# Performance work log

Measured on AMD Instinct MI355X. Metric: run time of the kernel, lower is better.

Reference implementation:

```python
import jax, jax.numpy as jnp
import numpy as np

OH, OW = 32, 32          # adaptive pool output size
NUM_KERNELS = 2
LATENT = 100             # latent_dims = [100, 100]
S = (OH // 2) * (OW // 2)  # in_spatial = 256


def adaptive_avg_pool(x, oh, ow):
    # exact-divisor adaptive avg pool == block mean
    B, C, H, W = x.shape
    return x.reshape(B, C, oh, H // oh, ow, W // ow).mean(axis=(3, 5))


def setup_inputs() -> dict:
    key = jax.random.key(0)
    k1, k2, k3, k4 = jax.random.split(key, 4)
    x = jax.random.normal(k1, (8, 512, 128, 128), dtype=jnp.float32)
    scale = 1.0 / np.sqrt(S)
    psi_w = jax.random.normal(k2, (NUM_KERNELS, S, LATENT), dtype=jnp.float32) * scale  # visible->latent proj
    phi_w = jax.random.normal(k3, (NUM_KERNELS, S, LATENT), dtype=jnp.float32) * scale  # latent->visible proj
    out_w = jax.random.normal(k4, (S, S), dtype=jnp.float32) * scale                    # output linear over spatial feats
    return {"x": x, "psi_w": psi_w, "phi_w": phi_w, "out_w": out_w}


def reference(x, psi_w, phi_w, out_w):
    B, C, H, W = x.shape
    # GAP: adaptive average pool to (OH, OW)
    xg = adaptive_avg_pool(x, OH, OW)                                   # [B,C,32,32]
    # internal 2x2 avg pool (accounts for in_spatial = h/2 * ceil(w/2))
    v = xg.reshape(B, C, OH // 2, 2, OW // 2, 2).mean(axis=(3, 5))
    v = v.reshape(B, C, S)                                              # channel nodes [B,C,S]
    # visible -> latent affinity (softmax over visible/channel nodes)
    A_v2l = jax.nn.softmax(jnp.einsum('bcs,ksd->bkdc', v, psi_w), axis=-1)  # [B,K,d1,C]
    z = jnp.einsum('bkdc,bcs->bkds', A_v2l, v).reshape(B, NUM_KERNELS * LATENT, S)  # [B,Kd1,S]
    # latent -> latent propagation on normalized features
    zn = z / (jnp.linalg.norm(z, axis=-1, keepdims=True) + 1e-6)
    G = jax.nn.softmax(jnp.einsum('bms,bns->bmn', zn, zn), axis=-1)     # [B,Kd1,Kd1]
    zp = jnp.einsum('bmn,bns->bms', G, z).reshape(B, NUM_KERNELS, LATENT, S)
    # latent -> visible affinity (softmax over latent nodes)
    A_l2v = jax.nn.softmax(jnp.einsum('bcs,ksd->bkcd', v, phi_w), axis=-1)  # [B,K,C,d2]
    out = jnp.einsum('bkcd,bkds->bcs', A_l2v, zp)                       # [B,C,S]
    out = jnp.einsum('bcs,st->bct', out, out_w)
    f = v + out                                                          # residual
    attn = jax.nn.sigmoid(f.mean(axis=-1))                               # [B,C]
    return attn[:, :, None, None]                                        # [B,C,1,1]
```

## Files before the change

kernel.cpp:

```cpp
#include <hip/hip_runtime.h>
#include <math.h>

constexpr int Bn = 8, Cn = 512, Sn = 256, Mn = 200, Ln = 100;

constexpr size_t OFF_V    = 0;
constexpr size_t OFF_Z    = OFF_V   + (size_t)Bn*Cn*Sn;
constexpr size_t OFF_INV  = OFF_Z   + (size_t)Bn*Mn*Sn;
constexpr size_t OFF_ZW   = OFF_INV + (size_t)Bn*Mn;
constexpr size_t OFF_ZPW  = OFF_ZW  + (size_t)Bn*Mn;
constexpr size_t OFF_WSUM = OFF_ZPW + (size_t)Bn*Mn;

template<int NW>
__device__ __forceinline__ float4 blk_max_f4(float4 x, float4* red) {
  #pragma unroll
  for (int o = 32; o; o >>= 1) {
    x.x = fmaxf(x.x, __shfl_xor(x.x, o));
    x.y = fmaxf(x.y, __shfl_xor(x.y, o));
    x.z = fmaxf(x.z, __shfl_xor(x.z, o));
    x.w = fmaxf(x.w, __shfl_xor(x.w, o));
  }
  __syncthreads();
  if ((threadIdx.x & 63) == 0) red[threadIdx.x >> 6] = x;
  __syncthreads();
  float4 r = red[0];
  #pragma unroll
  for (int w = 1; w < NW; ++w) {
    r.x = fmaxf(r.x, red[w].x); r.y = fmaxf(r.y, red[w].y);
    r.z = fmaxf(r.z, red[w].z); r.w = fmaxf(r.w, red[w].w);
  }
  return r;
}
template<int NW>
__device__ __forceinline__ float4 blk_sum_f4(float4 x, float4* red) {
  #pragma unroll
  for (int o = 32; o; o >>= 1) {
    x.x += __shfl_xor(x.x, o); x.y += __shfl_xor(x.y, o);
    x.z += __shfl_xor(x.z, o); x.w += __shfl_xor(x.w, o);
  }
  __syncthreads();
  if ((threadIdx.x & 63) == 0) red[threadIdx.x >> 6] = x;
  __syncthreads();
  float4 r = red[0];
  #pragma unroll
  for (int w = 1; w < NW; ++w) {
    r.x += red[w].x; r.y += red[w].y; r.z += red[w].z; r.w += red[w].w;
  }
  return r;
}

__global__ void __launch_bounds__(256) k_pool(const float* __restrict__ x,
                                              const float* __restrict__ ow,
                                              float* __restrict__ ws) {
  int t = threadIdx.x;
  if (blockIdx.x == 4096) {
    const float* row = ow + (size_t)t * Sn;
    float s = 0.f;
    for (int j = 0; j < Sn; j += 4) {
      float4 f = *(const float4*)(row + j);
      s += f.x + f.y + f.z + f.w;
    }
    ws[OFF_WSUM + t] = s;
    return;
  }
  int bc = blockIdx.x;
  const float* plane = x + (size_t)bc * 16384;
  float part[16];
  #pragma unroll
  for (int i = 0; i < 16; ++i) {
    float4 f = *(const float4*)(plane + i * 1024 + t * 4);
    part[i] = f.x + f.y + f.z + f.w;
  }
  __shared__ float lds[256][17];
  #pragma unroll
  for (int i = 0; i < 16; ++i) lds[t][i] = part[i];
  __syncthreads();
  int i = t >> 4, jj = t & 15;
  float s = 0.f;
  #pragma unroll
  for (int r = 0; r < 8; ++r)
    s += lds[32 * r + 2 * jj][i] + lds[32 * r + 2 * jj + 1][i];
  ws[OFF_V + (size_t)bc * 256 + t] = s * (1.0f / 64.0f);
}

__global__ void __launch_bounds__(512) k_psz(const float* __restrict__ psi,
                                             float* __restrict__ ws) {
  int b = blockIdx.y, g = blockIdx.x, t = threadIdx.x;
  int m0 = g * 8;
  __shared__ __align__(16) float pc[8][256];
  __shared__ __align__(16) float As[8][512];
  __shared__ __align__(16) float zpart[2][8][256];
  __shared__ float4 red4[8];
  const float* v = ws + OFF_V + (size_t)b * Cn * Sn;

  for (int e = t; e < 8 * 256; e += 512) {
    int mm = e >> 8, s = e & 255;
    int m = m0 + mm, k = m / Ln, d = m % Ln;
    pc[mm][s] = psi[(size_t)k * Sn * Ln + (size_t)s * Ln + d];
  }
  __syncthreads();

  float acc[8] = {0, 0, 0, 0, 0, 0, 0, 0};
  {
    const float* vp = v + (size_t)t * Sn;
    for (int s = 0; s < Sn; s += 4) {
      float4 vv = *(const float4*)(vp + s);
      #pragma unroll
      for (int mm = 0; mm < 8; ++mm) {
        float4 p = *(const float4*)&pc[mm][s];
        acc[mm] += vv.x * p.x + vv.y * p.y + vv.z * p.z + vv.w * p.w;
      }
    }
  }
  #pragma unroll
  for (int q = 0; q < 2; ++q) {
    float4 a = make_float4(acc[4*q], acc[4*q+1], acc[4*q+2], acc[4*q+3]);
    float4 mx = blk_max_f4<8>(a, red4);
    float4 e;
    e.x = expf(a.x - mx.x); e.y = expf(a.y - mx.y);
    e.z = expf(a.z - mx.z); e.w = expf(a.w - mx.w);
    float4 se = blk_sum_f4<8>(e, red4);
    As[4*q+0][t] = e.x / se.x;
    As[4*q+1][t] = e.y / se.y;
    As[4*q+2][t] = e.z / se.z;
    As[4*q+3][t] = e.w / se.w;
  }
  __syncthreads();

  int h = t >> 8, s2 = t & 255;
  float a2[8] = {0, 0, 0, 0, 0, 0, 0, 0};
  const float* vb = v + (size_t)h * 256 * Sn;
  for (int c = 0; c < 256; c += 4) {
    float v0 = vb[(size_t)(c + 0) * Sn + s2];
    float v1 = vb[(size_t)(c + 1) * Sn + s2];
    float v2 = vb[(size_t)(c + 2) * Sn + s2];
    float v3 = vb[(size_t)(c + 3) * Sn + s2];
    #pragma unroll
    for (int mm = 0; mm < 8; ++mm) {
      float4 aa = *(const float4*)&As[mm][h * 256 + c];
      a2[mm] += aa.x * v0 + aa.y * v1 + aa.z * v2 + aa.w * v3;
    }
  }
  #pragma unroll
  for (int mm = 0; mm < 8; ++mm) zpart[h][mm][s2] = a2[mm];
  __syncthreads();

  float zv[8] = {0, 0, 0, 0, 0, 0, 0, 0};
  float wsv = 0.f;
  if (t < 256) {
    wsv = ws[OFF_WSUM + t];
    float* zo = ws + OFF_Z + ((size_t)b * Mn + m0) * Sn;
    #pragma unroll
    for (int mm = 0; mm < 8; ++mm) {
      zv[mm] = zpart[0][mm][t] + zpart[1][mm][t];
      zo[(size_t)mm * Sn + t] = zv[mm];
    }
  }
  #pragma unroll
  for (int q = 0; q < 2; ++q) {
    float4 sq = make_float4(zv[4*q]*zv[4*q], zv[4*q+1]*zv[4*q+1],
                            zv[4*q+2]*zv[4*q+2], zv[4*q+3]*zv[4*q+3]);
    float4 n2 = blk_sum_f4<8>(sq, red4);
    float4 zw = blk_sum_f4<8>(make_float4(zv[4*q]*wsv, zv[4*q+1]*wsv,
                                          zv[4*q+2]*wsv, zv[4*q+3]*wsv), red4);
    if (t == 0) {
      float* inv = ws + OFF_INV + (size_t)b * Mn + m0 + 4*q;
      float* zwp = ws + OFF_ZW  + (size_t)b * Mn + m0 + 4*q;
      inv[0] = 1.0f / (sqrtf(n2.x) + 1e-6f); zwp[0] = zw.x;
      inv[1] = 1.0f / (sqrtf(n2.y) + 1e-6f); zwp[1] = zw.y;
      inv[2] = 1.0f / (sqrtf(n2.z) + 1e-6f); zwp[2] = zw.z;
      inv[3] = 1.0f / (sqrtf(n2.w) + 1e-6f); zwp[3] = zw.w;
    }
  }
}

__global__ void __launch_bounds__(256) k_g(float* __restrict__ ws) {
  int b = blockIdx.y, g = blockIdx.x, t = threadIdx.x;
  int m0 = g * 4;
  __shared__ __align__(16) float zl[4][256];
  __shared__ float invl[200], zwl[200];
  __shared__ float4 red4[4];
  const float* z = ws + OFF_Z + (size_t)b * Mn * Sn;
  #pragma unroll
  for (int mm = 0; mm < 4; ++mm) zl[mm][t] = z[(size_t)(m0 + mm) * Sn + t];
  if (t < Mn) {
    invl[t] = ws[OFF_INV + (size_t)b * Mn + t];
    zwl[t]  = ws[OFF_ZW  + (size_t)b * Mn + t];
  }
  __syncthreads();
  bool act = t < Mn;
  float dot[4] = {0, 0, 0, 0};
  if (act) {
    const float* zr = z + (size_t)t * Sn;
    for (int s = 0; s < Sn; s += 4) {
      float4 zz = *(const float4*)(zr + s);
      #pragma unroll
      for (int mm = 0; mm < 4; ++mm) {
        float4 zl4 = *(const float4*)&zl[mm][s];
        dot[mm] += zz.x * zl4.x + zz.y * zl4.y + zz.z * zl4.z + zz.w * zl4.w;
      }
    }
  }
  float4 val;
  val.x = act ? dot[0] * invl[m0 + 0] * invl[t] : -1e30f;
  val.y = act ? dot[1] * invl[m0 + 1] * invl[t] : -1e30f;
  val.z = act ? dot[2] * invl[m0 + 2] * invl[t] : -1e30f;
  val.w = act ? dot[3] * invl[m0 + 3] * invl[t] : -1e30f;
  float4 mx = blk_max_f4<4>(val, red4);
  float4 e;
  e.x = act ? expf(val.x - mx.x) : 0.f;
  e.y = act ? expf(val.y - mx.y) : 0.f;
  e.z = act ? expf(val.z - mx.z) : 0.f;
  e.w = act ? expf(val.w - mx.w) : 0.f;
  float4 se = blk_sum_f4<4>(e, red4);
  float zwn = act ? zwl[t] : 0.f;
  float4 sez = blk_sum_f4<4>(make_float4(e.x*zwn, e.y*zwn, e.z*zwn, e.w*zwn), red4);
  if (t == 0) {
    float* zp = ws + OFF_ZPW + (size_t)b * Mn + m0;
    zp[0] = sez.x / se.x; zp[1] = sez.y / se.y;
    zp[2] = sez.z / se.z; zp[3] = sez.w / se.w;
  }
}

__global__ void __launch_bounds__(256) k_out(const float* __restrict__ phi,
                                             float* __restrict__ out,
                                             float* __restrict__ ws) {
  int b = blockIdx.y, cg = blockIdx.x, t = threadIdx.x;
  int c0 = cg * 8;
  __shared__ __align__(16) float vl[8][256];
  __shared__ float zpl[200];
  __shared__ float t2l[16][104];
  __shared__ float resl[2][8];
  __shared__ float vsl[8];
  const float* v = ws + OFF_V + ((size_t)b * Cn + c0) * Sn;
  #pragma unroll
  for (int cc = 0; cc < 8; ++cc) vl[cc][t] = v[(size_t)cc * Sn + t];
  if (t < Mn) zpl[t] = ws[OFF_ZPW + (size_t)b * Mn + t];
  __syncthreads();
  int k = t >> 7, d = t & 127;
  int dd = d < Ln ? d : Ln - 1;
  const float* pp = phi + (size_t)k * Sn * Ln + dd;
  float acc[8] = {0, 0, 0, 0, 0, 0, 0, 0};
  for (int s = 0; s < Sn; s += 4) {
    float p0 = pp[(size_t)(s + 0) * Ln];
    float p1 = pp[(size_t)(s + 1) * Ln];
    float p2 = pp[(size_t)(s + 2) * Ln];
    float p3 = pp[(size_t)(s + 3) * Ln];
    #pragma unroll
    for (int cc = 0; cc < 8; ++cc) {
      float4 vv = *(const float4*)&vl[cc][s];
      acc[cc] += vv.x * p0 + vv.y * p1 + vv.z * p2 + vv.w * p3;
    }
  }
  if (d < Ln) {
    #pragma unroll
    for (int cc = 0; cc < 8; ++cc) t2l[k * 8 + cc][d] = acc[cc];
  }
  __syncthreads();
  int gg = t >> 4, l = t & 15;
  int k2 = gg >> 3, cc2 = gg & 7;
  float mx = -1e30f;
  for (int dq = l; dq < Ln; dq += 16) mx = fmaxf(mx, t2l[gg][dq]);
  #pragma unroll
  for (int o = 8; o; o >>= 1) mx = fmaxf(mx, __shfl_xor(mx, o));
  float se = 0.f, sez = 0.f;
  for (int dq = l; dq < Ln; dq += 16) {
    float e = expf(t2l[gg][dq] - mx);
    se += e;
    sez += e * zpl[k2 * Ln + dq];
  }
  #pragma unroll
  for (int o = 8; o; o >>= 1) { se += __shfl_xor(se, o); sez += __shfl_xor(sez, o); }
  float vs = 0.f;
  if (k2 == 0) {
    for (int i2 = 0; i2 < 16; ++i2) vs += vl[cc2][i2 * 16 + l];
    #pragma unroll
    for (int o = 8; o; o >>= 1) vs += __shfl_xor(vs, o);
    if (l == 0) vsl[cc2] = vs;
  }
  if (l == 0) resl[k2][cc2] = sez / se;
  __syncthreads();
  if (t < 8) {
    float f = (vsl[t] + resl[0][t] + resl[1][t]) * (1.0f / 256.0f);
    out[(size_t)b * Cn + c0 + t] = 1.0f / (1.0f + expf(-f));
  }
}

extern "C" void kernel_launch(void* const* d_in, const int* in_sizes, int n_in,
                              void* d_out, int out_size, void* d_ws, size_t ws_size,
                              hipStream_t stream) {
  const float* x   = (const float*)d_in[0];
  const float* psi = (const float*)d_in[1];
  const float* phi = (const float*)d_in[2];
  const float* ow  = (const float*)d_in[3];
  float* out = (float*)d_out;
  float* ws  = (float*)d_ws;

  hipLaunchKernelGGL(k_pool, dim3(4097),   dim3(256), 0, stream, x, ow, ws);
  hipLaunchKernelGGL(k_psz,  dim3(25, 8),  dim3(512), 0, stream, psi, ws);
  hipLaunchKernelGGL(k_g,    dim3(50, 8),  dim3(256), 0, stream, ws);
  hipLaunchKernelGGL(k_out,  dim3(64, 8),  dim3(256), 0, stream, phi, out, ws);
}
```

Before: 125.8 us.

## Add transposed v and z copies for coalesced loads and halve per-block work

The pooling kernel now also writes a transposed copy of v (S×C) and interleaves its block order across batches. k_psz writes a transposed z copy, and k_psz and k_g read these transposed buffers so each thread's loads are coalesced across lanes instead of strided per-thread rows. k_psz, k_g and k_out each handle half as many rows per block, doubling grid sizes for more parallelism. In exchange there are extra scattered global writes for the transposes and more total loads of the shared operands.

```diff
diff --git a/kernel.cpp b/kernel.cpp
--- a/kernel.cpp
+++ b/kernel.cpp
@@ -4,8 +4,10 @@
 constexpr int Bn = 8, Cn = 512, Sn = 256, Mn = 200, Ln = 100;
 
 constexpr size_t OFF_V    = 0;
-constexpr size_t OFF_Z    = OFF_V   + (size_t)Bn*Cn*Sn;
-constexpr size_t OFF_INV  = OFF_Z   + (size_t)Bn*Mn*Sn;
+constexpr size_t OFF_VT   = OFF_V   + (size_t)Bn*Cn*Sn;
+constexpr size_t OFF_Z    = OFF_VT  + (size_t)Bn*Sn*Cn;
+constexpr size_t OFF_ZT   = OFF_Z   + (size_t)Bn*Mn*Sn;
+constexpr size_t OFF_INV  = OFF_ZT  + (size_t)Bn*Sn*Mn;
 constexpr size_t OFF_ZW   = OFF_INV + (size_t)Bn*Mn;
 constexpr size_t OFF_ZPW  = OFF_ZW  + (size_t)Bn*Mn;
 constexpr size_t OFF_WSUM = OFF_ZPW + (size_t)Bn*Mn;
@@ -62,7 +64,8 @@
     ws[OFF_WSUM + t] = s;
     return;
   }
-  int bc = blockIdx.x;
+  int orig = blockIdx.x;
+  int bc = (orig & 7) * 512 + (orig >> 3);
   const float* plane = x + (size_t)bc * 16384;
   float part[16];
   #pragma unroll
@@ -79,145 +82,142 @@
   #pragma unroll
   for (int r = 0; r < 8; ++r)
     s += lds[32 * r + 2 * jj][i] + lds[32 * r + 2 * jj + 1][i];
-  ws[OFF_V + (size_t)bc * 256 + t] = s * (1.0f / 64.0f);
+  float val = s * (1.0f / 64.0f);
+  ws[OFF_V + (size_t)bc * 256 + t] = val;
+  int b = bc >> 9, c = bc & 511;
+  ws[OFF_VT + ((size_t)b * Sn + t) * Cn + c] = val;
 }
 
 __global__ void __launch_bounds__(512) k_psz(const float* __restrict__ psi,
                                              float* __restrict__ ws) {
   int b = blockIdx.y, g = blockIdx.x, t = threadIdx.x;
-  int m0 = g * 8;
-  __shared__ __align__(16) float pc[8][256];
-  __shared__ __align__(16) float As[8][512];
-  __shared__ __align__(16) float zpart[2][8][256];
+  int m0 = g * 4;
+  __shared__ __align__(16) float pc[4][256];
+  __shared__ __align__(16) float As[4][512];
+  __shared__ __align__(16) float zpart[2][4][256];
   __shared__ float4 red4[8];
-  const float* v = ws + OFF_V + (size_t)b * Cn * Sn;
-
-  for (int e = t; e < 8 * 256; e += 512) {
+  const float* v  = ws + OFF_V  + (size_t)b * Cn * Sn;
+  const float* vT = ws + OFF_VT + (size_t)b * Sn * Cn;
+
+  for (int e = t; e < 4 * 256; e += 512) {
     int mm = e >> 8, s = e & 255;
     int m = m0 + mm, k = m / Ln, d = m % Ln;
     pc[mm][s] = psi[(size_t)k * Sn * Ln + (size_t)s * Ln + d];
   }
   __syncthreads();
 
-  float acc[8] = {0, 0, 0, 0, 0, 0, 0, 0};
+  float acc[4] = {0, 0, 0, 0};
+  for (int s = 0; s < Sn; s += 4) {
+    float v0 = vT[(size_t)(s + 0) * Cn + t];
+    float v1 = vT[(size_t)(s + 1) * Cn + t];
+    float v2 = vT[(size_t)(s + 2) * Cn + t];
+    float v3 = vT[(size_t)(s + 3) * Cn + t];
+    #pragma unroll
+    for (int mm = 0; mm < 4; ++mm) {
+      float4 p = *(const float4*)&pc[mm][s];
+      acc[mm] += v0 * p.x + v1 * p.y + v2 * p.z + v3 * p.w;
+    }
+  }
   {
-    const float* vp = v + (size_t)t * Sn;
-    for (int s = 0; s < Sn; s += 4) {
-      float4 vv = *(const float4*)(vp + s);
-      #pragma unroll
-      for (int mm = 0; mm < 8; ++mm) {
-        float4 p = *(const float4*)&pc[mm][s];
-        acc[mm] += vv.x * p.x + vv.y * p.y + vv.z * p.z + vv.w * p.w;
-      }
-    }
-  }
-  #pragma unroll
-  for (int q = 0; q < 2; ++q) {
-    float4 a = make_float4(acc[4*q], acc[4*q+1], acc[4*q+2], acc[4*q+3]);
+    float4 a = make_float4(acc[0], acc[1], acc[2], acc[3]);
     float4 mx = blk_max_f4<8>(a, red4);
     float4 e;
     e.x = expf(a.x - mx.x); e.y = expf(a.y - mx.y);
     e.z = expf(a.z - mx.z); e.w = expf(a.w - mx.w);
     float4 se = blk_sum_f4<8>(e, red4);
-    As[4*q+0][t] = e.x / se.x;
-    As[4*q+1][t] = e.y / se.y;
-    As[4*q+2][t] = e.z / se.z;
-    As[4*q+3][t] = e.w / se.w;
+    As[0][t] = e.x / se.x;
+    As[1][t] = e.y / se.y;
+    As[2][t] = e.z / se.z;
+    As[3][t] = e.w / se.w;
   }
   __syncthreads();
 
   int h = t >> 8, s2 = t & 255;
-  float a2[8] = {0, 0, 0, 0, 0, 0, 0, 0};
+  float a2[4] = {0, 0, 0, 0};
   const float* vb = v + (size_t)h * 256 * Sn;
   for (int c = 0; c < 256; c += 4) {
-    float v0 = vb[(size_t)(c + 0) * Sn + s2];
-    float v1 = vb[(size_t)(c + 1) * Sn + s2];
-    float v2 = vb[(size_t)(c + 2) * Sn + s2];
-    float v3 = vb[(size_t)(c + 3) * Sn + s2];
-    #pragma unroll
-    for (int mm = 0; mm < 8; ++mm) {
+    float w0 = vb[(size_t)(c + 0) * Sn + s2];
+    float w1 = vb[(size_t)(c + 1) * Sn + s2];
+    float w2 = vb[(size_t)(c + 2) * Sn + s2];
+    float w3 = vb[(size_t)(c + 3) * Sn + s2];
+    #pragma unroll
+    for (int mm = 0; mm < 4; ++mm) {
       float4 aa = *(const float4*)&As[mm][h * 256 + c];
-      a2[mm] += aa.x * v0 + aa.y * v1 + aa.z * v2 + aa.w * v3;
-    }
-  }
-  #pragma unroll
-  for (int mm = 0; mm < 8; ++mm) zpart[h][mm][s2] = a2[mm];
-  __syncthreads();
-
-  float zv[8] = {0, 0, 0, 0, 0, 0, 0, 0};
+      a2[mm] += aa.x * w0 + aa.y * w1 + aa.z * w2 + aa.w * w3;
+    }
+  }
+  #pragma unroll
+  for (int mm = 0; mm < 4; ++mm) zpart[h][mm][s2] = a2[mm];
+  __syncthreads();
+
+  float zv[4] = {0, 0, 0, 0};
   float wsv = 0.f;
   if (t < 256) {
     wsv = ws[OFF_WSUM + t];
     float* zo = ws + OFF_Z + ((size_t)b * Mn + m0) * Sn;
     #pragma unroll
-    for (int mm = 0; mm < 8; ++mm) {
+    for (int mm = 0; mm < 4; ++mm) {
       zv[mm] = zpart[0][mm][t] + zpart[1][mm][t];
       zo[(size_t)mm * Sn + t] = zv[mm];
     }
-  }
-  #pragma unroll
-  for (int q = 0; q < 2; ++q) {
-    float4 sq = make_float4(zv[4*q]*zv[4*q], zv[4*q+1]*zv[4*q+1],
-                            zv[4*q+2]*zv[4*q+2], zv[4*q+3]*zv[4*q+3]);
-    float4 n2 = blk_sum_f4<8>(sq, red4);
-    float4 zw = blk_sum_f4<8>(make_float4(zv[4*q]*wsv, zv[4*q+1]*wsv,
-                                          zv[4*q+2]*wsv, zv[4*q+3]*wsv), red4);
-    if (t == 0) {
-      float* inv = ws + OFF_INV + (size_t)b * Mn + m0 + 4*q;
-      float* zwp = ws + OFF_ZW  + (size_t)b * Mn + m0 + 4*q;
-      inv[0] = 1.0f / (sqrtf(n2.x) + 1e-6f); zwp[0] = zw.x;
-      inv[1] = 1.0f / (sqrtf(n2.y) + 1e-6f); zwp[1] = zw.y;
-      inv[2] = 1.0f / (sqrtf(n2.z) + 1e-6f); zwp[2] = zw.z;
-      inv[3] = 1.0f / (sqrtf(n2.w) + 1e-6f); zwp[3] = zw.w;
-    }
+    *(float4*)&ws[OFF_ZT + ((size_t)b * Sn + t) * Mn + m0] =
+        make_float4(zv[0], zv[1], zv[2], zv[3]);
+  }
+  float4 n2 = blk_sum_f4<8>(make_float4(zv[0]*zv[0], zv[1]*zv[1],
+                                        zv[2]*zv[2], zv[3]*zv[3]), red4);
+  float4 zw = blk_sum_f4<8>(make_float4(zv[0]*wsv, zv[1]*wsv,
+                                        zv[2]*wsv, zv[3]*wsv), red4);
+  if (t == 0) {
+    float* inv = ws + OFF_INV + (size_t)b * Mn + m0;
+    float* zwp = ws + OFF_ZW  + (size_t)b * Mn + m0;
+    inv[0] = 1.0f / (sqrtf(n2.x) + 1e-6f); zwp[0] = zw.x;
+    inv[1] = 1.0f / (sqrtf(n2.y) + 1e-6f); zwp[1] = zw.y;
+    inv[2] = 1.0f / (sqrtf(n2.z) + 1e-6f); zwp[2] = zw.z;
+    inv[3] = 1.0f / (sqrtf(n2.w) + 1e-6f); zwp[3] = zw.w;
   }
 }
 
 __global__ void __launch_bounds__(256) k_g(float* __restrict__ ws) {
   int b = blockIdx.y, g = blockIdx.x, t = threadIdx.x;
-  int m0 = g * 4;
-  __shared__ __align__(16) float zl[4][256];
+  int m0 = g * 2;
+  __shared__ __align__(16) float zl[2][256];
   __shared__ float invl[200], zwl[200];
   __shared__ float4 red4[4];
-  const float* z = ws + OFF_Z + (size_t)b * Mn * Sn;
-  #pragma unroll
-  for (int mm = 0; mm < 4; ++mm) zl[mm][t] = z[(size_t)(m0 + mm) * Sn + t];
+  const float* z  = ws + OFF_Z  + (size_t)b * Mn * Sn;
+  const float* zT = ws + OFF_ZT + (size_t)b * Sn * Mn;
+  zl[0][t] = z[(size_t)(m0 + 0) * Sn + t];
+  zl[1][t] = z[(size_t)(m0 + 1) * Sn + t];
   if (t < Mn) {
     invl[t] = ws[OFF_INV + (size_t)b * Mn + t];
     zwl[t]  = ws[OFF_ZW  + (size_t)b * Mn + t];
   }
   __syncthreads();
   bool act = t < Mn;
-  float dot[4] = {0, 0, 0, 0};
+  float d0 = 0.f, d1 = 0.f;
   if (act) {
-    const float* zr = z + (size_t)t * Sn;
     for (int s = 0; s < Sn; s += 4) {
-      float4 zz = *(const float4*)(zr + s);
-      #pragma unroll
-      for (int mm = 0; mm < 4; ++mm) {
-        float4 zl4 = *(const float4*)&zl[mm][s];
-        dot[mm] += zz.x * zl4.x + zz.y * zl4.y + zz.z * zl4.z + zz.w * zl4.w;
-      }
+      float z0 = zT[(size_t)(s + 0) * Mn + t];
+      float z1 = zT[(size_t)(s + 1) * Mn + t];
+      float z2 = zT[(size_t)(s + 2) * Mn + t];
+      float z3 = zT[(size_t)(s + 3) * Mn + t];
+      d0 += z0 * zl[0][s] + z1 * zl[0][s+1] + z2 * zl[0][s+2] + z3 * zl[0][s+3];
+      d1 += z0 * zl[1][s] + z1 * zl[1][s+1] + z2 * zl[1][s+2] + z3 * zl[1][s+3];
     }
   }
   float4 val;
-  val.x = act ? dot[0] * invl[m0 + 0] * invl[t] : -1e30f;
-  val.y = act ? dot[1] * invl[m0 + 1] * invl[t] : -1e30f;
-  val.z = act ? dot[2] * invl[m0 + 2] * invl[t] : -1e30f;
-  val.w = act ? dot[3] * invl[m0 + 3] * invl[t] : -1e30f;
+  val.x = act ? d0 * invl[m0 + 0] * invl[t] : -1e30f;
+  val.y = act ? d1 * invl[m0 + 1] * invl[t] : -1e30f;
+  val.z = -1e30f; val.w = -1e30f;
   float4 mx = blk_max_f4<4>(val, red4);
-  float4 e;
-  e.x = act ? expf(val.x - mx.x) : 0.f;
-  e.y = act ? expf(val.y - mx.y) : 0.f;
-  e.z = act ? expf(val.z - mx.z) : 0.f;
-  e.w = act ? expf(val.w - mx.w) : 0.f;
-  float4 se = blk_sum_f4<4>(e, red4);
+  float ex = act ? expf(val.x - mx.x) : 0.f;
+  float ey = act ? expf(val.y - mx.y) : 0.f;
+  float4 se = blk_sum_f4<4>(make_float4(ex, ey, 0.f, 0.f), red4);
   float zwn = act ? zwl[t] : 0.f;
-  float4 sez = blk_sum_f4<4>(make_float4(e.x*zwn, e.y*zwn, e.z*zwn, e.w*zwn), red4);
+  float4 sez = blk_sum_f4<4>(make_float4(ex * zwn, ey * zwn, 0.f, 0.f), red4);
   if (t == 0) {
     float* zp = ws + OFF_ZPW + (size_t)b * Mn + m0;
-    zp[0] = sez.x / se.x; zp[1] = sez.y / se.y;
-    zp[2] = sez.z / se.z; zp[3] = sez.w / se.w;
+    zp[0] = sez.x / se.x;
+    zp[1] = sez.y / se.y;
   }
 }
 
@@ -225,61 +225,61 @@
                                              float* __restrict__ out,
                                              float* __restrict__ ws) {
   int b = blockIdx.y, cg = blockIdx.x, t = threadIdx.x;
-  int c0 = cg * 8;
-  __shared__ __align__(16) float vl[8][256];
+  int c0 = cg * 4;
+  __shared__ __align__(16) float vl[4][256];
   __shared__ float zpl[200];
-  __shared__ float t2l[16][104];
-  __shared__ float resl[2][8];
-  __shared__ float vsl[8];
+  __shared__ float t2l[8][104];
+  __shared__ float resl[2][4];
+  __shared__ float vsl[4];
   const float* v = ws + OFF_V + ((size_t)b * Cn + c0) * Sn;
   #pragma unroll
-  for (int cc = 0; cc < 8; ++cc) vl[cc][t] = v[(size_t)cc * Sn + t];
+  for (int cc = 0; cc < 4; ++cc) vl[cc][t] = v[(size_t)cc * Sn + t];
   if (t < Mn) zpl[t] = ws[OFF_ZPW + (size_t)b * Mn + t];
   __syncthreads();
   int k = t >> 7, d = t & 127;
   int dd = d < Ln ? d : Ln - 1;
   const float* pp = phi + (size_t)k * Sn * Ln + dd;
-  float acc[8] = {0, 0, 0, 0, 0, 0, 0, 0};
+  float acc[4] = {0, 0, 0, 0};
   for (int s = 0; s < Sn; s += 4) {
     float p0 = pp[(size_t)(s + 0) * Ln];
     float p1 = pp[(size_t)(s + 1) * Ln];
     float p2 = pp[(size_t)(s + 2) * Ln];
     float p3 = pp[(size_t)(s + 3) * Ln];
     #pragma unroll
-    for (int cc = 0; cc < 8; ++cc) {
+    for (int cc = 0; cc < 4; ++cc) {
       float4 vv = *(const float4*)&vl[cc][s];
       acc[cc] += vv.x * p0 + vv.y * p1 + vv.z * p2 + vv.w * p3;
     }
   }
   if (d < Ln) {
     #pragma unroll
-    for (int cc = 0; cc < 8; ++cc) t2l[k * 8 + cc][d] = acc[cc];
-  }
-  __syncthreads();
-  int gg = t >> 4, l = t & 15;
-  int k2 = gg >> 3, cc2 = gg & 7;
+    for (int cc = 0; cc < 4; ++cc) t2l[k * 4 + cc][d] = acc[cc];
+  }
+  __syncthreads();
+  int gg = t >> 5, l = t & 31;
+  int k2 = gg >> 2, cc2 = gg & 3;
   float mx = -1e30f;
-  for (int dq = l; dq < Ln; dq += 16) mx = fmaxf(mx, t2l[gg][dq]);
-  #pragma unroll
-  for (int o = 8; o; o >>= 1) mx = fmaxf(mx, __shfl_xor(mx, o));
+  for (int dq = l; dq < Ln; dq += 32) mx = fmaxf(mx, t2l[gg][dq]);
+  #pragma unroll
+  for (int o = 16; o; o >>= 1) mx = fmaxf(mx, __shfl_xor(mx, o));
   float se = 0.f, sez = 0.f;
-  for (int dq = l; dq < Ln; dq += 16) {
+  for (int dq = l; dq < Ln; dq += 32) {
     float e = expf(t2l[gg][dq] - mx);
     se += e;
     sez += e * zpl[k2 * Ln + dq];
   }
   #pragma unroll
-  for (int o = 8; o; o >>= 1) { se += __shfl_xor(se, o); sez += __shfl_xor(sez, o); }
+  for (int o = 16; o; o >>= 1) { se += __shfl_xor(se, o); sez += __shfl_xor(sez, o); }
   float vs = 0.f;
   if (k2 == 0) {
-    for (int i2 = 0; i2 < 16; ++i2) vs += vl[cc2][i2 * 16 + l];
-    #pragma unroll
-    for (int o = 8; o; o >>= 1) vs += __shfl_xor(vs, o);
+    for (int i2 = 0; i2 < 8; ++i2) vs += vl[cc2][i2 * 32 + l];
+    #pragma unroll
+    for (int o = 16; o; o >>= 1) vs += __shfl_xor(vs, o);
     if (l == 0) vsl[cc2] = vs;
   }
   if (l == 0) resl[k2][cc2] = sez / se;
   __syncthreads();
-  if (t < 8) {
+  if (t < 4) {
     float f = (vsl[t] + resl[0][t] + resl[1][t]) * (1.0f / 256.0f);
     out[(size_t)b * Cn + c0 + t] = 1.0f / (1.0f + expf(-f));
   }
@@ -295,8 +295,8 @@
   float* out = (float*)d_out;
   float* ws  = (float*)d_ws;
 
-  hipLaunchKernelGGL(k_pool, dim3(4097),   dim3(256), 0, stream, x, ow, ws);
-  hipLaunchKernelGGL(k_psz,  dim3(25, 8),  dim3(512), 0, stream, psi, ws);
-  hipLaunchKernelGGL(k_g,    dim3(50, 8),  dim3(256), 0, stream, ws);
-  hipLaunchKernelGGL(k_out,  dim3(64, 8),  dim3(256), 0, stream, phi, out, ws);
-}
+  hipLaunchKernelGGL(k_pool, dim3(4097),    dim3(256), 0, stream, x, ow, ws);
+  hipLaunchKernelGGL(k_psz,  dim3(50, 8),   dim3(512), 0, stream, psi, ws);
+  hipLaunchKernelGGL(k_g,    dim3(100, 8),  dim3(256), 0, stream, ws);
+  hipLaunchKernelGGL(k_out,  dim3(128, 8),  dim3(256), 0, stream, phi, out, ws);
+}
```

New measurement: 128.2 us. About the same (+1.9%).

## Fuse four stages into one cooperative persistent kernel with grid syncs

Applied to the files above, without the earlier changes.

Merges the pool, psi-softmax/z, latent-softmax and output stages into a single cooperative kernel of 1024 blocks that separates the phases with grid.sync(). The pool phase now loops four planes per block, and the later stages are retiled to 256-thread blocks with 4 rows or channels each. The goal is to remove launch gaps and inter-kernel drains and to keep the grid resident on the GPU. In exchange it pays grid-barrier overhead, leaves blocks idle in the phases that use only 400 blocks, and runs the bandwidth-heavy pool stage with fewer in-flight blocks.

```diff
diff --git a/kernel.cpp b/kernel.cpp
--- a/kernel.cpp
+++ b/kernel.cpp
@@ -1,5 +1,8 @@
 #include <hip/hip_runtime.h>
+#include <hip/hip_cooperative_groups.h>
 #include <math.h>
+
+namespace cg = cooperative_groups;
 
 constexpr int Bn = 8, Cn = 512, Sn = 256, Mn = 200, Ln = 100;
 
@@ -10,7 +13,13 @@
 constexpr size_t OFF_ZPW  = OFF_ZW  + (size_t)Bn*Mn;
 constexpr size_t OFF_WSUM = OFF_ZPW + (size_t)Bn*Mn;
 
-template<int NW>
+struct PoolS { float lds[256][9]; };
+struct PszS  { float pc[4][256]; float As[4][512]; };
+struct GS    { float zl[4][256]; float invl[200]; float zwl[200]; };
+struct OutS  { float vl[4][256]; float zpl[200]; float t2l[8][104];
+               float resl[2][4]; float vsl[4]; };
+union ShU { PoolS p; PszS z; GS g; OutS o; };
+
 __device__ __forceinline__ float4 blk_max_f4(float4 x, float4* red) {
   #pragma unroll
   for (int o = 32; o; o >>= 1) {
@@ -24,13 +33,12 @@
   __syncthreads();
   float4 r = red[0];
   #pragma unroll
-  for (int w = 1; w < NW; ++w) {
+  for (int w = 1; w < 4; ++w) {
     r.x = fmaxf(r.x, red[w].x); r.y = fmaxf(r.y, red[w].y);
     r.z = fmaxf(r.z, red[w].z); r.w = fmaxf(r.w, red[w].w);
   }
   return r;
 }
-template<int NW>
 __device__ __forceinline__ float4 blk_sum_f4(float4 x, float4* red) {
   #pragma unroll
   for (int o = 32; o; o >>= 1) {
@@ -42,17 +50,47 @@
   __syncthreads();
   float4 r = red[0];
   #pragma unroll
-  for (int w = 1; w < NW; ++w) {
+  for (int w = 1; w < 4; ++w) {
     r.x += red[w].x; r.y += red[w].y; r.z += red[w].z; r.w += red[w].w;
   }
   return r;
 }
 
-__global__ void __launch_bounds__(256) k_pool(const float* __restrict__ x,
-                                              const float* __restrict__ ow,
-                                              float* __restrict__ ws) {
-  int t = threadIdx.x;
-  if (blockIdx.x == 4096) {
+__device__ void dev_pool(const float* __restrict__ x, const float* __restrict__ ow,
+                         float* __restrict__ ws, PoolS& sh, int bl, int t) {
+  #pragma unroll 1
+  for (int rp = 0; rp < 4; ++rp) {
+    int bc = bl + rp * 1024;
+    const float* plane = x + (size_t)bc * 16384;
+    float part[16];
+    #pragma unroll
+    for (int i = 0; i < 16; ++i) {
+      float4 f = *(const float4*)(plane + i * 1024 + t * 4);
+      part[i] = f.x + f.y + f.z + f.w;
+    }
+    int i = t >> 4, jj = t & 15;
+    float s = 0.f;
+    __syncthreads();
+    #pragma unroll
+    for (int q = 0; q < 8; ++q) sh.lds[t][q] = part[q];
+    __syncthreads();
+    if (i < 8) {
+      #pragma unroll
+      for (int r = 0; r < 8; ++r)
+        s += sh.lds[32 * r + 2 * jj][i] + sh.lds[32 * r + 2 * jj + 1][i];
+    }
+    __syncthreads();
+    #pragma unroll
+    for (int q = 0; q < 8; ++q) sh.lds[t][q] = part[8 + q];
+    __syncthreads();
+    if (i >= 8) {
+      #pragma unroll
+      for (int r = 0; r < 8; ++r)
+        s += sh.lds[32 * r + 2 * jj][i - 8] + sh.lds[32 * r + 2 * jj + 1][i - 8];
+    }
+    ws[OFF_V + (size_t)bc * 256 + t] = s * (1.0f / 64.0f);
+  }
+  if (bl == 0) {
     const float* row = ow + (size_t)t * Sn;
     float s = 0.f;
     for (int j = 0; j < Sn; j += 4) {
@@ -60,131 +98,89 @@
       s += f.x + f.y + f.z + f.w;
     }
     ws[OFF_WSUM + t] = s;
-    return;
-  }
-  int bc = blockIdx.x;
-  const float* plane = x + (size_t)bc * 16384;
-  float part[16];
-  #pragma unroll
-  for (int i = 0; i < 16; ++i) {
-    float4 f = *(const float4*)(plane + i * 1024 + t * 4);
-    part[i] = f.x + f.y + f.z + f.w;
-  }
-  __shared__ float lds[256][17];
-  #pragma unroll
-  for (int i = 0; i < 16; ++i) lds[t][i] = part[i];
-  __syncthreads();
-  int i = t >> 4, jj = t & 15;
-  float s = 0.f;
-  #pragma unroll
-  for (int r = 0; r < 8; ++r)
-    s += lds[32 * r + 2 * jj][i] + lds[32 * r + 2 * jj + 1][i];
-  ws[OFF_V + (size_t)bc * 256 + t] = s * (1.0f / 64.0f);
-}
-
-__global__ void __launch_bounds__(512) k_psz(const float* __restrict__ psi,
-                                             float* __restrict__ ws) {
-  int b = blockIdx.y, g = blockIdx.x, t = threadIdx.x;
-  int m0 = g * 8;
-  __shared__ __align__(16) float pc[8][256];
-  __shared__ __align__(16) float As[8][512];
-  __shared__ __align__(16) float zpart[2][8][256];
-  __shared__ float4 red4[8];
+  }
+}
+
+__device__ void dev_psz(const float* __restrict__ psi, float* __restrict__ ws,
+                        PszS& sh, float4* red4, int bl, int t) {
+  if (bl >= 400) return;
+  int b = bl / 50, g = bl % 50, m0 = g * 4;
   const float* v = ws + OFF_V + (size_t)b * Cn * Sn;
-
-  for (int e = t; e < 8 * 256; e += 512) {
+  for (int e = t; e < 4 * 256; e += 256) {
     int mm = e >> 8, s = e & 255;
     int m = m0 + mm, k = m / Ln, d = m % Ln;
-    pc[mm][s] = psi[(size_t)k * Sn * Ln + (size_t)s * Ln + d];
-  }
-  __syncthreads();
-
-  float acc[8] = {0, 0, 0, 0, 0, 0, 0, 0};
-  {
-    const float* vp = v + (size_t)t * Sn;
-    for (int s = 0; s < Sn; s += 4) {
-      float4 vv = *(const float4*)(vp + s);
-      #pragma unroll
-      for (int mm = 0; mm < 8; ++mm) {
-        float4 p = *(const float4*)&pc[mm][s];
-        acc[mm] += vv.x * p.x + vv.y * p.y + vv.z * p.z + vv.w * p.w;
-      }
-    }
-  }
-  #pragma unroll
-  for (int q = 0; q < 2; ++q) {
-    float4 a = make_float4(acc[4*q], acc[4*q+1], acc[4*q+2], acc[4*q+3]);
-    float4 mx = blk_max_f4<8>(a, red4);
-    float4 e;
-    e.x = expf(a.x - mx.x); e.y = expf(a.y - mx.y);
-    e.z = expf(a.z - mx.z); e.w = expf(a.w - mx.w);
-    float4 se = blk_sum_f4<8>(e, red4);
-    As[4*q+0][t] = e.x / se.x;
-    As[4*q+1][t] = e.y / se.y;
-    As[4*q+2][t] = e.z / se.z;
-    As[4*q+3][t] = e.w / se.w;
-  }
-  __syncthreads();
-
-  int h = t >> 8, s2 = t & 255;
-  float a2[8] = {0, 0, 0, 0, 0, 0, 0, 0};
-  const float* vb = v + (size_t)h * 256 * Sn;
-  for (int c = 0; c < 256; c += 4) {
-    float v0 = vb[(size_t)(c + 0) * Sn + s2];
-    float v1 = vb[(size_t)(c + 1) * Sn + s2];
-    float v2 = vb[(size_t)(c + 2) * Sn + s2];
-    float v3 = vb[(size_t)(c + 3) * Sn + s2];
-    #pragma unroll
-    for (int mm = 0; mm < 8; ++mm) {
-      float4 aa = *(const float4*)&As[mm][h * 256 + c];
-      a2[mm] += aa.x * v0 + aa.y * v1 + aa.z * v2 + aa.w * v3;
-    }
-  }
-  #pragma unroll
-  for (int mm = 0; mm < 8; ++mm) zpart[h][mm][s2] = a2[mm];
-  __syncthreads();
-
-  float zv[8] = {0, 0, 0, 0, 0, 0, 0, 0};
-  float wsv = 0.f;
-  if (t < 256) {
-    wsv = ws[OFF_WSUM + t];
-    float* zo = ws + OFF_Z + ((size_t)b * Mn + m0) * Sn;
-    #pragma unroll
-    for (int mm = 0; mm < 8; ++mm) {
-      zv[mm] = zpart[0][mm][t] + zpart[1][mm][t];
-      zo[(size_t)mm * Sn + t] = zv[mm];
-    }
-  }
-  #pragma unroll
-  for (int q = 0; q < 2; ++q) {
-    float4 sq = make_float4(zv[4*q]*zv[4*q], zv[4*q+1]*zv[4*q+1],
-                            zv[4*q+2]*zv[4*q+2], zv[4*q+3]*zv[4*q+3]);
-    float4 n2 = blk_sum_f4<8>(sq, red4);
-    float4 zw = blk_sum_f4<8>(make_float4(zv[4*q]*wsv, zv[4*q+1]*wsv,
-                                          zv[4*q+2]*wsv, zv[4*q+3]*wsv), red4);
-    if (t == 0) {
-      float* inv = ws + OFF_INV + (size_t)b * Mn + m0 + 4*q;
-      float* zwp = ws + OFF_ZW  + (size_t)b * Mn + m0 + 4*q;
-      inv[0] = 1.0f / (sqrtf(n2.x) + 1e-6f); zwp[0] = zw.x;
-      inv[1] = 1.0f / (sqrtf(n2.y) + 1e-6f); zwp[1] = zw.y;
-      inv[2] = 1.0f / (sqrtf(n2.z) + 1e-6f); zwp[2] = zw.z;
-      inv[3] = 1.0f / (sqrtf(n2.w) + 1e-6f); zwp[3] = zw.w;
-    }
-  }
-}
-
-__global__ void __launch_bounds__(256) k_g(float* __restrict__ ws) {
-  int b = blockIdx.y, g = blockIdx.x, t = threadIdx.x;
-  int m0 = g * 4;
-  __shared__ __align__(16) float zl[4][256];
-  __shared__ float invl[200], zwl[200];
-  __shared__ float4 red4[4];
+    sh.pc[mm][s] = psi[(size_t)k * Sn * Ln + (size_t)s * Ln + d];
+  }
+  __syncthreads();
+  float acc[2][4];
+  #pragma unroll
+  for (int mm = 0; mm < 4; ++mm) { acc[0][mm] = 0.f; acc[1][mm] = 0.f; }
+  const float* vp0 = v + (size_t)t * Sn;
+  const float* vp1 = v + (size_t)(t + 256) * Sn;
+  for (int s = 0; s < Sn; s += 4) {
+    float4 v0 = *(const float4*)(vp0 + s);
+    float4 v1 = *(const float4*)(vp1 + s);
+    #pragma unroll
+    for (int mm = 0; mm < 4; ++mm) {
+      float4 p = *(const float4*)&sh.pc[mm][s];
+      acc[0][mm] += v0.x * p.x + v0.y * p.y + v0.z * p.z + v0.w * p.w;
+      acc[1][mm] += v1.x * p.x + v1.y * p.y + v1.z * p.z + v1.w * p.w;
+    }
+  }
+  float4 a = make_float4(fmaxf(acc[0][0], acc[1][0]), fmaxf(acc[0][1], acc[1][1]),
+                         fmaxf(acc[0][2], acc[1][2]), fmaxf(acc[0][3], acc[1][3]));
+  float4 mx = blk_max_f4(a, red4);
+  float e00 = expf(acc[0][0] - mx.x), e10 = expf(acc[1][0] - mx.x);
+  float e01 = expf(acc[0][1] - mx.y), e11 = expf(acc[1][1] - mx.y);
+  float e02 = expf(acc[0][2] - mx.z), e12 = expf(acc[1][2] - mx.z);
+  float e03 = expf(acc[0][3] - mx.w), e13 = expf(acc[1][3] - mx.w);
+  float4 se = blk_sum_f4(make_float4(e00 + e10, e01 + e11, e02 + e12, e03 + e13),
+                         red4);
+  sh.As[0][t] = e00 / se.x; sh.As[0][t + 256] = e10 / se.x;
+  sh.As[1][t] = e01 / se.y; sh.As[1][t + 256] = e11 / se.y;
+  sh.As[2][t] = e02 / se.z; sh.As[2][t + 256] = e12 / se.z;
+  sh.As[3][t] = e03 / se.w; sh.As[3][t + 256] = e13 / se.w;
+  __syncthreads();
+  float zv[4] = {0, 0, 0, 0};
+  for (int c = 0; c < Cn; c += 4) {
+    float w0 = v[(size_t)(c + 0) * Sn + t];
+    float w1 = v[(size_t)(c + 1) * Sn + t];
+    float w2 = v[(size_t)(c + 2) * Sn + t];
+    float w3 = v[(size_t)(c + 3) * Sn + t];
+    #pragma unroll
+    for (int mm = 0; mm < 4; ++mm) {
+      float4 aa = *(const float4*)&sh.As[mm][c];
+      zv[mm] += aa.x * w0 + aa.y * w1 + aa.z * w2 + aa.w * w3;
+    }
+  }
+  float wsv = ws[OFF_WSUM + t];
+  float* zo = ws + OFF_Z + ((size_t)b * Mn + m0) * Sn;
+  #pragma unroll
+  for (int mm = 0; mm < 4; ++mm) zo[(size_t)mm * Sn + t] = zv[mm];
+  float4 n2 = blk_sum_f4(make_float4(zv[0]*zv[0], zv[1]*zv[1],
+                                     zv[2]*zv[2], zv[3]*zv[3]), red4);
+  float4 zw = blk_sum_f4(make_float4(zv[0]*wsv, zv[1]*wsv,
+                                     zv[2]*wsv, zv[3]*wsv), red4);
+  if (t == 0) {
+    float* inv = ws + OFF_INV + (size_t)b * Mn + m0;
+    float* zwp = ws + OFF_ZW  + (size_t)b * Mn + m0;
+    inv[0] = 1.0f / (sqrtf(n2.x) + 1e-6f); zwp[0] = zw.x;
+    inv[1] = 1.0f / (sqrtf(n2.y) + 1e-6f); zwp[1] = zw.y;
+    inv[2] = 1.0f / (sqrtf(n2.z) + 1e-6f); zwp[2] = zw.z;
+    inv[3] = 1.0f / (sqrtf(n2.w) + 1e-6f); zwp[3] = zw.w;
+  }
+}
+
+__device__ void dev_g(float* __restrict__ ws, GS& sh, float4* red4, int bl, int t) {
+  if (bl >= 400) return;
+  int b = bl / 50, g2 = bl % 50, m0 = g2 * 4;
   const float* z = ws + OFF_Z + (size_t)b * Mn * Sn;
   #pragma unroll
-  for (int mm = 0; mm < 4; ++mm) zl[mm][t] = z[(size_t)(m0 + mm) * Sn + t];
+  for (int mm = 0; mm < 4; ++mm)
+    sh.zl[mm][t] = z[(size_t)(m0 + mm) * Sn + t];
   if (t < Mn) {
-    invl[t] = ws[OFF_INV + (size_t)b * Mn + t];
-    zwl[t]  = ws[OFF_ZW  + (size_t)b * Mn + t];
+    sh.invl[t] = ws[OFF_INV + (size_t)b * Mn + t];
+    sh.zwl[t]  = ws[OFF_ZW  + (size_t)b * Mn + t];
   }
   __syncthreads();
   bool act = t < Mn;
@@ -195,25 +191,25 @@
       float4 zz = *(const float4*)(zr + s);
       #pragma unroll
       for (int mm = 0; mm < 4; ++mm) {
-        float4 zl4 = *(const float4*)&zl[mm][s];
+        float4 zl4 = *(const float4*)&sh.zl[mm][s];
         dot[mm] += zz.x * zl4.x + zz.y * zl4.y + zz.z * zl4.z + zz.w * zl4.w;
       }
     }
   }
   float4 val;
-  val.x = act ? dot[0] * invl[m0 + 0] * invl[t] : -1e30f;
-  val.y = act ? dot[1] * invl[m0 + 1] * invl[t] : -1e30f;
-  val.z = act ? dot[2] * invl[m0 + 2] * invl[t] : -1e30f;
-  val.w = act ? dot[3] * invl[m0 + 3] * invl[t] : -1e30f;
-  float4 mx = blk_max_f4<4>(val, red4);
+  val.x = act ? dot[0] * sh.invl[m0 + 0] * sh.invl[t] : -1e30f;
+  val.y = act ? dot[1] * sh.invl[m0 + 1] * sh.invl[t] : -1e30f;
+  val.z = act ? dot[2] * sh.invl[m0 + 2] * sh.invl[t] : -1e30f;
+  val.w = act ? dot[3] * sh.invl[m0 + 3] * sh.invl[t] : -1e30f;
+  float4 mx = blk_max_f4(val, red4);
   float4 e;
   e.x = act ? expf(val.x - mx.x) : 0.f;
   e.y = act ? expf(val.y - mx.y) : 0.f;
   e.z = act ? expf(val.z - mx.z) : 0.f;
   e.w = act ? expf(val.w - mx.w) : 0.f;
-  float4 se = blk_sum_f4<4>(e, red4);
-  float zwn = act ? zwl[t] : 0.f;
-  float4 sez = blk_sum_f4<4>(make_float4(e.x*zwn, e.y*zwn, e.z*zwn, e.w*zwn), red4);
+  float4 se = blk_sum_f4(e, red4);
+  float zwn = act ? sh.zwl[t] : 0.f;
+  float4 sez = blk_sum_f4(make_float4(e.x*zwn, e.y*zwn, e.z*zwn, e.w*zwn), red4);
   if (t == 0) {
     float* zp = ws + OFF_ZPW + (size_t)b * Mn + m0;
     zp[0] = sez.x / se.x; zp[1] = sez.y / se.y;
@@ -221,68 +217,100 @@
   }
 }
 
-__global__ void __launch_bounds__(256) k_out(const float* __restrict__ phi,
-                                             float* __restrict__ out,
-                                             float* __restrict__ ws) {
-  int b = blockIdx.y, cg = blockIdx.x, t = threadIdx.x;
-  int c0 = cg * 8;
-  __shared__ __align__(16) float vl[8][256];
-  __shared__ float zpl[200];
-  __shared__ float t2l[16][104];
-  __shared__ float resl[2][8];
-  __shared__ float vsl[8];
+__device__ void dev_out(const float* __restrict__ phi, float* __restrict__ out,
+                        float* __restrict__ ws, OutS& sh, int bl, int t) {
+  int b = bl >> 7, cgrp = bl & 127, c0 = cgrp * 4;
   const float* v = ws + OFF_V + ((size_t)b * Cn + c0) * Sn;
   #pragma unroll
-  for (int cc = 0; cc < 8; ++cc) vl[cc][t] = v[(size_t)cc * Sn + t];
-  if (t < Mn) zpl[t] = ws[OFF_ZPW + (size_t)b * Mn + t];
+  for (int cc = 0; cc < 4; ++cc) sh.vl[cc][t] = v[(size_t)cc * Sn + t];
+  if (t < Mn) sh.zpl[t] = ws[OFF_ZPW + (size_t)b * Mn + t];
   __syncthreads();
   int k = t >> 7, d = t & 127;
   int dd = d < Ln ? d : Ln - 1;
   const float* pp = phi + (size_t)k * Sn * Ln + dd;
-  float acc[8] = {0, 0, 0, 0, 0, 0, 0, 0};
+  float acc[4] = {0, 0, 0, 0};
   for (int s = 0; s < Sn; s += 4) {
     float p0 = pp[(size_t)(s + 0) * Ln];
     float p1 = pp[(size_t)(s + 1) * Ln];
     float p2 = pp[(size_t)(s + 2) * Ln];
     float p3 = pp[(size_t)(s + 3) * Ln];
     #pragma unroll
-    for (int cc = 0; cc < 8; ++cc) {
-      float4 vv = *(const float4*)&vl[cc][s];
+    for (int cc = 0; cc < 4; ++cc) {
+      float4 vv = *(const float4*)&sh.vl[cc][s];
       acc[cc] += vv.x * p0 + vv.y * p1 + vv.z * p2 + vv.w * p3;
     }
   }
   if (d < Ln) {
     #pragma unroll
-    for (int cc = 0; cc < 8; ++cc) t2l[k * 8 + cc][d] = acc[cc];
-  }
-  __syncthreads();
-  int gg = t >> 4, l = t & 15;
-  int k2 = gg >> 3, cc2 = gg & 7;
+    for (int cc = 0; cc < 4; ++cc) sh.t2l[k * 4 + cc][d] = acc[cc];
+  }
+  __syncthreads();
+  int gg = t >> 5, l = t & 31;
+  int k2 = gg >> 2, cc2 = gg & 3;
   float mx = -1e30f;
-  for (int dq = l; dq < Ln; dq += 16) mx = fmaxf(mx, t2l[gg][dq]);
-  #pragma unroll
-  for (int o = 8; o; o >>= 1) mx = fmaxf(mx, __shfl_xor(mx, o));
+  for (int dq = l; dq < Ln; dq += 32) mx = fmaxf(mx, sh.t2l[gg][dq]);
+  #pragma unroll
+  for (int o = 16; o; o >>= 1) mx = fmaxf(mx, __shfl_xor(mx, o));
   float se = 0.f, sez = 0.f;
-  for (int dq = l; dq < Ln; dq += 16) {
-    float e = expf(t2l[gg][dq] - mx);
+  for (int dq = l; dq < Ln; dq += 32) {
+    float e = expf(sh.t2l[gg][dq] - mx);
     se += e;
-    sez += e * zpl[k2 * Ln + dq];
-  }
-  #pragma unroll
-  for (int o = 8; o; o >>= 1) { se += __shfl_xor(se, o); sez += __shfl_xor(sez, o); }
+    sez += e * sh.zpl[k2 * Ln + dq];
+  }
+  #pragma unroll
+  for (int o = 16; o; o >>= 1) { se += __shfl_xor(se, o); sez += __shfl_xor(sez, o); }
   float vs = 0.f;
   if (k2 == 0) {
-    for (int i2 = 0; i2 < 16; ++i2) vs += vl[cc2][i2 * 16 + l];
-    #pragma unroll
-    for (int o = 8; o; o >>= 1) vs += __shfl_xor(vs, o);
-    if (l == 0) vsl[cc2] = vs;
-  }
-  if (l == 0) resl[k2][cc2] = sez / se;
-  __syncthreads();
-  if (t < 8) {
-    float f = (vsl[t] + resl[0][t] + resl[1][t]) * (1.0f / 256.0f);
+    for (int i2 = 0; i2 < 8; ++i2) vs += sh.vl[cc2][i2 * 32 + l];
+    #pragma unroll
+    for (int o = 16; o; o >>= 1) vs += __shfl_xor(vs, o);
+    if (l == 0) sh.vsl[cc2] = vs;
+  }
+  if (l == 0) sh.resl[k2][cc2] = sez / se;
+  __syncthreads();
+  if (t < 4) {
+    float f = (sh.vsl[t] + sh.resl[0][t] + sh.resl[1][t]) * (1.0f / 256.0f);
     out[(size_t)b * Cn + c0 + t] = 1.0f / (1.0f + expf(-f));
   }
+}
+
+__global__ void __launch_bounds__(256, 4)
+k_all(const float* __restrict__ x, const float* __restrict__ psi,
+      const float* __restrict__ phi, const float* __restrict__ ow,
+      float* __restrict__ out, float* __restrict__ ws) {
+  cg::grid_group grid = cg::this_grid();
+  __shared__ ShU sh;
+  __shared__ float4 red4[4];
+  int t = threadIdx.x, bl = blockIdx.x;
+  dev_pool(x, ow, ws, sh.p, bl, t);
+  grid.sync();
+  dev_psz(psi, ws, sh.z, red4, bl, t);
+  grid.sync();
+  dev_g(ws, sh.g, red4, bl, t);
+  grid.sync();
+  dev_out(phi, out, ws, sh.o, bl, t);
+}
+
+__global__ void __launch_bounds__(256) k_pool_f(const float* __restrict__ x,
+                                                const float* __restrict__ ow,
+                                                float* __restrict__ ws) {
+  __shared__ PoolS sh;
+  dev_pool(x, ow, ws, sh, blockIdx.x, threadIdx.x);
+}
+__global__ void __launch_bounds__(256) k_psz_f(const float* __restrict__ psi,
+                                               float* __restrict__ ws) {
+  __shared__ PszS sh; __shared__ float4 red4[4];
+  dev_psz(psi, ws, sh, red4, blockIdx.x, threadIdx.x);
+}
+__global__ void __launch_bounds__(256) k_g_f(float* __restrict__ ws) {
+  __shared__ GS sh; __shared__ float4 red4[4];
+  dev_g(ws, sh, red4, blockIdx.x, threadIdx.x);
+}
+__global__ void __launch_bounds__(256) k_out_f(const float* __restrict__ phi,
+                                               float* __restrict__ out,
+                                               float* __restrict__ ws) {
+  __shared__ OutS sh;
+  dev_out(phi, out, ws, sh, blockIdx.x, threadIdx.x);
 }
 
 extern "C" void kernel_launch(void* const* d_in, const int* in_sizes, int n_in,
@@ -295,8 +323,20 @@
   float* out = (float*)d_out;
   float* ws  = (float*)d_ws;
 
-  hipLaunchKernelGGL(k_pool, dim3(4097),   dim3(256), 0, stream, x, ow, ws);
-  hipLaunchKernelGGL(k_psz,  dim3(25, 8),  dim3(512), 0, stream, psi, ws);
-  hipLaunchKernelGGL(k_g,    dim3(50, 8),  dim3(256), 0, stream, ws);
-  hipLaunchKernelGGL(k_out,  dim3(64, 8),  dim3(256), 0, stream, phi, out, ws);
-}
+  int maxBlk = 0;
+  hipError_t qerr = hipOccupancyMaxActiveBlocksPerMultiprocessor(
+      &maxBlk, (const void*)k_all, 256, 0);
+  bool coop = (qerr == hipSuccess && maxBlk >= 4);
+
+  if (coop) {
+    void* args[] = {(void*)&x, (void*)&psi, (void*)&phi, (void*)&ow,
+                    (void*)&out, (void*)&ws};
+    hipError_t lerr = hipLaunchCooperativeKernel(
+        (void*)k_all, dim3(1024), dim3(256), args, 0, stream);
+    if (lerr == hipSuccess) return;
+  }
+  hipLaunchKernelGGL(k_pool_f, dim3(1024),  dim3(256), 0, stream, x, ow, ws);
+  hipLaunchKernelGGL(k_psz_f,  dim3(400),   dim3(256), 0, stream, psi, ws);
+  hipLaunchKernelGGL(k_g_f,    dim3(400),   dim3(256), 0, stream, ws);
+  hipLaunchKernelGGL(k_out_f,  dim3(1024),  dim3(256), 0, stream, phi, out, ws);
+}
```

Measured after the change: 176.6 us. +40.4%, slower.
